# Kernel tuning notes

Hardware: AMD Instinct MI355X
Metric: run time of the kernel (lower is better)

The kernel has to match this reference:

```python
import jax, jax.numpy as jnp
import numpy as np

B, H, W = 64, 512, 512          # batch, image height/width
BH, BW = 8, 8                   # block_size
K = 256                         # n_blocks (codebook size)
L = BH * BW                     # block_len = 64
HT, WT = H // BH, W // BW       # tiles per axis
T = HT * WT                     # tiles_per_img = 4096
BETA = 35.0


def _unfold(img):
    # img: (B, 1, H, W) -> patches (B, T, L), matching torch.nn.Unfold
    # with kernel=stride=(BH,BW): tiles row-major, patch flattened (kh, kw).
    x = img.reshape(B, 1, HT, BH, WT, BW)
    x = x.transpose(0, 2, 4, 1, 3, 5)          # (B, HT, WT, 1, BH, BW)
    return x.reshape(B, T, L)


def _fold(patches):
    # patches: (B, T, L) -> img (B, 1, H, W); exact inverse of _unfold
    # (non-overlapping, so Fold is pure reassembly, no accumulation).
    x = patches.reshape(B, HT, WT, 1, BH, BW)
    x = x.transpose(0, 3, 1, 4, 2, 5)          # (B, 1, HT, BH, WT, BW)
    return x.reshape(B, 1, H, W)


def setup_inputs() -> dict:
    key = jax.random.key(0)
    k1, k2 = jax.random.split(key)
    target_img = jax.random.uniform(k1, (B, 1, H, W), dtype=jnp.float32)
    # Learned codebook parameter (Haar-ish init in the original; values
    # don't change the math being tested).
    blocks = jax.random.uniform(k2, (K, BH, BW), dtype=jnp.float32)
    return {"target_img": target_img, "blocks": blocks}


def reference(target_img, blocks):
    patches = _unfold(target_img).reshape(B * T, L)   # (N, L), N = B*T
    codes = blocks.reshape(K, L)                      # (K, L)

    # Squared distances ||a - b||^2 via the expanded form to avoid
    # materializing the (N, K, L) difference tensor.
    a2 = jnp.sum(patches * patches, axis=-1, keepdims=True)   # (N, 1)
    b2 = jnp.sum(codes * codes, axis=-1)                      # (K,)
    ab = patches @ codes.T                                    # (N, K)
    sqerr = a2 - 2.0 * ab + b2                                # (N, K)

    block_weights = jax.nn.softmax(-BETA * sqerr, axis=-1)    # (N, K)
    uf_reconstructed = block_weights @ codes                  # (N, L)

    reconstructed = _fold(uf_reconstructed.reshape(B, T, L))  # (B,1,H,W)
    choice_penalty = jnp.mean(
        jnp.minimum(block_weights, 1.0 - block_weights)) * K
    return reconstructed, choice_penalty
```

## Files before the change

kernel.cpp:

```cpp
#include <hip/hip_runtime.h>


namespace {
constexpr int   HALF   = 128;
constexpr float BETA_C = 35.0f;
constexpr float TAU    = 1e-6f;
constexpr int   NPATCH = 64 * 64 * 64;
constexpr size_t IMG_ELEMS = (size_t)64 * 512 * 512;
}

template <int H>
__device__ __forceinline__ void stage_codes(float* sC, const float* __restrict__ blk,
                                            int tid) {
#pragma unroll 8
  for (int i = 0; i < 32; ++i) {
    int f = i * 256 + tid;
    int kl = f >> 6;
    int d = f & 63;
    float v = blk[H * 8192 + f];
    sC[d * HALF + (kl ^ ((d & 15) << 1))] = v;
  }
}

template <int H>
__device__ __forceinline__ void gemm_half(float (&acc)[16][4], float (&b2acc)[4],
                                          const float* sC, const float* sP,
                                          int lane, int wave) {
  const float* prBase = &sP[wave * 16];
#pragma unroll 4
  for (int d = 0; d < 64; ++d) {
    const float2 c2 = *reinterpret_cast<const float2*>(
        &sC[d * HALF + 2 * (lane ^ (d & 15))]);
    b2acc[2 * H]     += c2.x * c2.x;
    b2acc[2 * H + 1] += c2.y * c2.y;
    const float* pr = prBase + d * 64;
#pragma unroll
    for (int pg = 0; pg < 4; ++pg) {
      const float4 pa = *reinterpret_cast<const float4*>(pr + pg * 4);
      acc[pg * 4 + 0][2 * H]     += pa.x * c2.x;
      acc[pg * 4 + 0][2 * H + 1] += pa.x * c2.y;
      acc[pg * 4 + 1][2 * H]     += pa.y * c2.x;
      acc[pg * 4 + 1][2 * H + 1] += pa.y * c2.y;
      acc[pg * 4 + 2][2 * H]     += pa.z * c2.x;
      acc[pg * 4 + 2][2 * H + 1] += pa.z * c2.y;
      acc[pg * 4 + 3][2 * H]     += pa.w * c2.x;
      acc[pg * 4 + 3][2 * H + 1] += pa.w * c2.y;
    }
  }
}

__global__ __launch_bounds__(256, 3) void recon_kernel(
    const float* __restrict__ img, const float* __restrict__ blk,
    float* __restrict__ out, float* __restrict__ penAcc) {
  __shared__ float sC[64 * HALF];
  __shared__ float sP[64 * 64];

  const int tid = threadIdx.x;
  const int lane = tid & 63;
  const int wave = tid >> 6;
  const int b = blockIdx.x >> 6;
  const int ht = blockIdx.x & 63;

  const float* imgBase = img + (size_t)b * (512 * 512) + (size_t)(ht * 8) * 512;
#pragma unroll
  for (int i = 0; i < 4; ++i) {
    int f4 = i * 256 + tid;
    int row = f4 >> 7;
    int c4 = f4 & 127;
    float4 v = reinterpret_cast<const float4*>(imgBase + row * 512)[c4];
    int col = c4 * 4;
    int wt = col >> 3;
    int dbase = row * 8 + (col & 7);
    sP[(dbase + 0) * 64 + wt] = v.x;
    sP[(dbase + 1) * 64 + wt] = v.y;
    sP[(dbase + 2) * 64 + wt] = v.z;
    sP[(dbase + 3) * 64 + wt] = v.w;
  }
  stage_codes<0>(sC, blk, tid);
  __syncthreads();

  float acc[16][4];
  float b2acc[4] = {0.f, 0.f, 0.f, 0.f};
#pragma unroll
  for (int p = 0; p < 16; ++p)
#pragma unroll
    for (int j = 0; j < 4; ++j) acc[p][j] = 0.f;

  gemm_half<0>(acc, b2acc, sC, sP, lane, wave);
  __syncthreads();
  stage_codes<1>(sC, blk, tid);
  __syncthreads();
  gemm_half<1>(acc, b2acc, sC, sP, lane, wave);

  float pen = 0.f;
  const int wtBase = wave * 16;
  const int kh = lane >> 3, kw = lane & 7;
  float* outRowBase =
      out + (size_t)b * (512 * 512) + (size_t)(ht * 8 + kh) * 512 + kw;

  for (int p = 0; p < 16; ++p) {
    float l0 = BETA_C * (2.f * acc[p][0] - b2acc[0]);
    float l1 = BETA_C * (2.f * acc[p][1] - b2acc[1]);
    float l2 = BETA_C * (2.f * acc[p][2] - b2acc[2]);
    float l3 = BETA_C * (2.f * acc[p][3] - b2acc[3]);
    float m = fmaxf(fmaxf(l0, l1), fmaxf(l2, l3));
#pragma unroll
    for (int off = 32; off >= 1; off >>= 1)
      m = fmaxf(m, __shfl_xor(m, off, 64));
    float e0 = __expf(l0 - m), e1 = __expf(l1 - m);
    float e2 = __expf(l2 - m), e3 = __expf(l3 - m);
    float s = (e0 + e1) + (e2 + e3);
#pragma unroll
    for (int off = 32; off >= 1; off >>= 1) s += __shfl_xor(s, off, 64);
    float inv = 1.0f / s;
    float w0 = e0 * inv, w1 = e1 * inv, w2 = e2 * inv, w3 = e3 * inv;
    pen += fmaxf(2.f * w0 - 1.f, 0.f) + fmaxf(2.f * w1 - 1.f, 0.f) +
           fmaxf(2.f * w2 - 1.f, 0.f) + fmaxf(2.f * w3 - 1.f, 0.f);

    bool flag = (w0 > TAU) || (w1 > TAU) || (w2 > TAU) || (w3 > TAU);
    unsigned long long mask = __ballot(flag ? 1 : 0);
    float r = 0.f;
    while (mask) {
      int L = __builtin_ctzll(mask);
      mask &= (mask - 1);
      float q0 = __shfl(w0, L, 64);
      float q1 = __shfl(w1, L, 64);
      float q2 = __shfl(w2, L, 64);
      float q3 = __shfl(w3, L, 64);
      const float* cb = blk + (2 * L) * 64 + lane;
      if (q0 > TAU) r = fmaf(q0, cb[0], r);
      if (q1 > TAU) r = fmaf(q1, cb[64], r);
      if (q2 > TAU) r = fmaf(q2, cb[HALF * 64], r);
      if (q3 > TAU) r = fmaf(q3, cb[HALF * 64 + 64], r);
    }
    outRowBase[(wtBase + p) * 8] = r;
  }

#pragma unroll
  for (int off = 32; off >= 1; off >>= 1) pen += __shfl_xor(pen, off, 64);
  if (lane == 0) atomicAdd(penAcc, pen);
}

__global__ void finalize_kernel(float* penSlot) {
  *penSlot = 1.0f - (*penSlot) * (1.0f / (float)NPATCH);
}

extern "C" void kernel_launch(void* const* d_in, const int* in_sizes, int n_in,
                              void* d_out, int out_size, void* d_ws, size_t ws_size,
                              hipStream_t stream) {
  const float* img = (const float*)d_in[0];
  const float* blk = (const float*)d_in[1];
  float* out = (float*)d_out;
  float* penSlot = out + IMG_ELEMS;

  hipMemsetAsync(penSlot, 0, sizeof(float), stream);
  recon_kernel<<<dim3(4096), dim3(256), 0, stream>>>(img, blk, out, penSlot);
  finalize_kernel<<<dim3(1), dim3(1), 0, stream>>>(penSlot);
}
```

Before: 406.5 us.

## Compute patch-codebook distances with split-bf16 MFMA and stage output through LDS

Replaces the scalar FP32 FMA distance GEMM with bf16 MFMA 16x16x32 instructions, splitting both operands into hi and lo bf16 parts to keep close to FP32 accuracy (hi*hi, lo*hi, hi*lo and lo*lo terms). A small pre-kernel packs the codebook into hi/lo bf16 fragments and precomputes the code norms, removing that work from each block. Softmax weights are written to shared memory as bf16, and the reconstructed patches are staged in shared memory so the image is written with coalesced float4 stores. The risk is reduced precision from storing the weights in bf16, plus extra LDS traffic and synchronisation.

```diff
diff --git a/kernel.cpp b/kernel.cpp
--- a/kernel.cpp
+++ b/kernel.cpp
@@ -1,148 +1,238 @@
 #include <hip/hip_runtime.h>
-
+#include <hip/hip_fp16.h>
+
+
+typedef short short8 __attribute__((ext_vector_type(8)));
+typedef float floatx4 __attribute__((ext_vector_type(4)));
 
 namespace {
-constexpr int   HALF   = 128;
 constexpr float BETA_C = 35.0f;
 constexpr float TAU    = 1e-6f;
-constexpr int   NPATCH = 64 * 64 * 64;
+constexpr float INV_N  = 1.0f / 262144.0f;
 constexpr size_t IMG_ELEMS = (size_t)64 * 512 * 512;
-}
-
-template <int H>
-__device__ __forceinline__ void stage_codes(float* sC, const float* __restrict__ blk,
-                                            int tid) {
-#pragma unroll 8
-  for (int i = 0; i < 32; ++i) {
-    int f = i * 256 + tid;
-    int kl = f >> 6;
-    int d = f & 63;
-    float v = blk[H * 8192 + f];
-    sC[d * HALF + (kl ^ ((d & 15) << 1))] = v;
-  }
-}
-
-template <int H>
-__device__ __forceinline__ void gemm_half(float (&acc)[16][4], float (&b2acc)[4],
-                                          const float* sC, const float* sP,
-                                          int lane, int wave) {
-  const float* prBase = &sP[wave * 16];
-#pragma unroll 4
-  for (int d = 0; d < 64; ++d) {
-    const float2 c2 = *reinterpret_cast<const float2*>(
-        &sC[d * HALF + 2 * (lane ^ (d & 15))]);
-    b2acc[2 * H]     += c2.x * c2.x;
-    b2acc[2 * H + 1] += c2.y * c2.y;
-    const float* pr = prBase + d * 64;
-#pragma unroll
-    for (int pg = 0; pg < 4; ++pg) {
-      const float4 pa = *reinterpret_cast<const float4*>(pr + pg * 4);
-      acc[pg * 4 + 0][2 * H]     += pa.x * c2.x;
-      acc[pg * 4 + 0][2 * H + 1] += pa.x * c2.y;
-      acc[pg * 4 + 1][2 * H]     += pa.y * c2.x;
-      acc[pg * 4 + 1][2 * H + 1] += pa.y * c2.y;
-      acc[pg * 4 + 2][2 * H]     += pa.z * c2.x;
-      acc[pg * 4 + 2][2 * H + 1] += pa.z * c2.y;
-      acc[pg * 4 + 3][2 * H]     += pa.w * c2.x;
-      acc[pg * 4 + 3][2 * H + 1] += pa.w * c2.y;
-    }
-  }
+constexpr int WB   = 0;
+constexpr int WA_H = 9216;
+constexpr int WA_L = 11264;
+constexpr int WW   = 0;
+constexpr int WR   = 8448;
+constexpr int NWORDS = 13312;
+}
+
+__device__ __forceinline__ unsigned short f2bf(float x) {
+  unsigned u = __float_as_uint(x);
+  return (unsigned short)((u + 0x7FFFu + ((u >> 16) & 1u)) >> 16);
+}
+__device__ __forceinline__ float bf2f(unsigned short h) {
+  return __uint_as_float((unsigned)h << 16);
+}
+__device__ __forceinline__ unsigned pack2(unsigned short lo, unsigned short hi) {
+  return (unsigned)lo | ((unsigned)hi << 16);
+}
+
+__global__ void pack_codes(const float* __restrict__ blk,
+                           unsigned* __restrict__ wsBh,
+                           unsigned* __restrict__ wsBl,
+                           float* __restrict__ wsB2) {
+  const int c = threadIdx.x;
+  const float* src = blk + c * 64;
+  float b2 = 0.f;
+#pragma unroll
+  for (int g = 0; g < 8; ++g) {
+#pragma unroll
+    for (int t = 0; t < 4; ++t) {
+      float v0 = src[g * 8 + 2 * t], v1 = src[g * 8 + 2 * t + 1];
+      b2 += v0 * v0 + v1 * v1;
+      unsigned short h0 = f2bf(v0), h1 = f2bf(v1);
+      unsigned short l0 = f2bf(v0 - bf2f(h0)), l1 = f2bf(v1 - bf2f(h1));
+      wsBh[(c * 8 + g) * 4 + t] = pack2(h0, h1);
+      wsBl[(c * 8 + g) * 4 + t] = pack2(l0, l1);
+    }
+  }
+  wsB2[c] = b2;
 }
 
 __global__ __launch_bounds__(256, 3) void recon_kernel(
     const float* __restrict__ img, const float* __restrict__ blk,
-    float* __restrict__ out, float* __restrict__ penAcc) {
-  __shared__ float sC[64 * HALF];
-  __shared__ float sP[64 * 64];
+    const unsigned* __restrict__ wsBh, const unsigned* __restrict__ wsBl,
+    const float* __restrict__ wsB2, float* __restrict__ out,
+    float* __restrict__ penAcc) {
+  __shared__ unsigned sMem[NWORDS];
+  float* sMemF = reinterpret_cast<float*>(sMem);
 
   const int tid = threadIdx.x;
   const int lane = tid & 63;
   const int wave = tid >> 6;
   const int b = blockIdx.x >> 6;
   const int ht = blockIdx.x & 63;
-
+  const int c15 = lane & 15;
+  const int q = lane >> 4;
+
+  {
+    const uint4* src = reinterpret_cast<const uint4*>(wsBh);
+#pragma unroll
+    for (int i = 0; i < 8; ++i) {
+      int j = i * 256 + tid;
+      *reinterpret_cast<uint4*>(&sMem[WB + (j + (j >> 3)) * 4]) = src[j];
+    }
+  }
   const float* imgBase = img + (size_t)b * (512 * 512) + (size_t)(ht * 8) * 512;
 #pragma unroll
   for (int i = 0; i < 4; ++i) {
     int f4 = i * 256 + tid;
-    int row = f4 >> 7;
-    int c4 = f4 & 127;
+    int row = f4 >> 7, c4 = f4 & 127;
     float4 v = reinterpret_cast<const float4*>(imgBase + row * 512)[c4];
-    int col = c4 * 4;
-    int wt = col >> 3;
-    int dbase = row * 8 + (col & 7);
-    sP[(dbase + 0) * 64 + wt] = v.x;
-    sP[(dbase + 1) * 64 + wt] = v.y;
-    sP[(dbase + 2) * 64 + wt] = v.z;
-    sP[(dbase + 3) * 64 + wt] = v.w;
-  }
-  stage_codes<0>(sC, blk, tid);
-  __syncthreads();
-
-  float acc[16][4];
-  float b2acc[4] = {0.f, 0.f, 0.f, 0.f};
-#pragma unroll
-  for (int p = 0; p < 16; ++p)
-#pragma unroll
-    for (int j = 0; j < 4; ++j) acc[p][j] = 0.f;
-
-  gemm_half<0>(acc, b2acc, sC, sP, lane, wave);
-  __syncthreads();
-  stage_codes<1>(sC, blk, tid);
-  __syncthreads();
-  gemm_half<1>(acc, b2acc, sC, sP, lane, wave);
+    int wt = c4 >> 1, hw = c4 & 1;
+    unsigned short h0 = f2bf(v.x), h1 = f2bf(v.y), h2 = f2bf(v.z), h3 = f2bf(v.w);
+    unsigned short l0 = f2bf(v.x - bf2f(h0)), l1 = f2bf(v.y - bf2f(h1));
+    unsigned short l2 = f2bf(v.z - bf2f(h2)), l3 = f2bf(v.w - bf2f(h3));
+    int base = wt * 32 + row * 4 + hw * 2;
+    *reinterpret_cast<uint2*>(&sMem[WA_H + base]) =
+        make_uint2(pack2(h0, h1), pack2(h2, h3));
+    *reinterpret_cast<uint2*>(&sMem[WA_L + base]) =
+        make_uint2(pack2(l0, l1), pack2(l2, l3));
+  }
+  __syncthreads();
+
+  const int patch = wave * 16 + c15;
+  short8 ah[2], al[2];
+#pragma unroll
+  for (int s = 0; s < 2; ++s) {
+    int base = patch * 32 + (4 * s + q) * 4;
+    ah[s] = *reinterpret_cast<const short8*>(&sMem[WA_H + base]);
+    al[s] = *reinterpret_cast<const short8*>(&sMem[WA_L + base]);
+  }
+
+  floatx4 acc[16];
+#pragma unroll
+  for (int n = 0; n < 16; ++n) acc[n] = (floatx4){0.f, 0.f, 0.f, 0.f};
+
+#pragma unroll
+  for (int n = 0; n < 16; ++n) {
+    const unsigned* pb = &sMem[WB + (144 * n + 9 * c15 + q) * 4];
+    short8 b0 = *reinterpret_cast<const short8*>(pb);
+    short8 b1 = *reinterpret_cast<const short8*>(pb + 16);
+    acc[n] = __builtin_amdgcn_mfma_f32_16x16x32_bf16(ah[0], b0, acc[n], 0, 0, 0);
+    acc[n] = __builtin_amdgcn_mfma_f32_16x16x32_bf16(al[0], b0, acc[n], 0, 0, 0);
+    acc[n] = __builtin_amdgcn_mfma_f32_16x16x32_bf16(ah[1], b1, acc[n], 0, 0, 0);
+    acc[n] = __builtin_amdgcn_mfma_f32_16x16x32_bf16(al[1], b1, acc[n], 0, 0, 0);
+  }
+  __syncthreads();
+  {
+    const uint4* src = reinterpret_cast<const uint4*>(wsBl);
+#pragma unroll
+    for (int i = 0; i < 8; ++i) {
+      int j = i * 256 + tid;
+      *reinterpret_cast<uint4*>(&sMem[WB + (j + (j >> 3)) * 4]) = src[j];
+    }
+  }
+  __syncthreads();
+#pragma unroll
+  for (int n = 0; n < 16; ++n) {
+    const unsigned* pb = &sMem[WB + (144 * n + 9 * c15 + q) * 4];
+    short8 b0 = *reinterpret_cast<const short8*>(pb);
+    short8 b1 = *reinterpret_cast<const short8*>(pb + 16);
+    acc[n] = __builtin_amdgcn_mfma_f32_16x16x32_bf16(ah[0], b0, acc[n], 0, 0, 0);
+    acc[n] = __builtin_amdgcn_mfma_f32_16x16x32_bf16(al[0], b0, acc[n], 0, 0, 0);
+    acc[n] = __builtin_amdgcn_mfma_f32_16x16x32_bf16(ah[1], b1, acc[n], 0, 0, 0);
+    acc[n] = __builtin_amdgcn_mfma_f32_16x16x32_bf16(al[1], b1, acc[n], 0, 0, 0);
+  }
+
+#pragma unroll
+  for (int n = 0; n < 16; ++n) {
+    float b2v = wsB2[16 * n + c15];
+#pragma unroll
+    for (int r = 0; r < 4; ++r)
+      acc[n][r] = fmaf(2.0f * BETA_C, acc[n][r], -BETA_C * b2v);
+  }
+  float mx[4], sm[4];
+#pragma unroll
+  for (int r = 0; r < 4; ++r) {
+    float m = acc[0][r];
+#pragma unroll
+    for (int n = 1; n < 16; ++n) m = fmaxf(m, acc[n][r]);
+#pragma unroll
+    for (int off = 1; off <= 8; off <<= 1) m = fmaxf(m, __shfl_xor(m, off, 64));
+    mx[r] = m;
+    sm[r] = 0.f;
+  }
+#pragma unroll
+  for (int n = 0; n < 16; ++n)
+#pragma unroll
+    for (int r = 0; r < 4; ++r) {
+      acc[n][r] = __expf(acc[n][r] - mx[r]);
+      sm[r] += acc[n][r];
+    }
+#pragma unroll
+  for (int r = 0; r < 4; ++r) {
+#pragma unroll
+    for (int off = 1; off <= 8; off <<= 1) sm[r] += __shfl_xor(sm[r], off, 64);
+    sm[r] = 1.0f / sm[r];
+  }
+
+  __syncthreads();
 
   float pen = 0.f;
-  const int wtBase = wave * 16;
-  const int kh = lane >> 3, kw = lane & 7;
-  float* outRowBase =
-      out + (size_t)b * (512 * 512) + (size_t)(ht * 8 + kh) * 512 + kw;
-
-  for (int p = 0; p < 16; ++p) {
-    float l0 = BETA_C * (2.f * acc[p][0] - b2acc[0]);
-    float l1 = BETA_C * (2.f * acc[p][1] - b2acc[1]);
-    float l2 = BETA_C * (2.f * acc[p][2] - b2acc[2]);
-    float l3 = BETA_C * (2.f * acc[p][3] - b2acc[3]);
-    float m = fmaxf(fmaxf(l0, l1), fmaxf(l2, l3));
-#pragma unroll
-    for (int off = 32; off >= 1; off >>= 1)
-      m = fmaxf(m, __shfl_xor(m, off, 64));
-    float e0 = __expf(l0 - m), e1 = __expf(l1 - m);
-    float e2 = __expf(l2 - m), e3 = __expf(l3 - m);
-    float s = (e0 + e1) + (e2 + e3);
-#pragma unroll
-    for (int off = 32; off >= 1; off >>= 1) s += __shfl_xor(s, off, 64);
-    float inv = 1.0f / s;
-    float w0 = e0 * inv, w1 = e1 * inv, w2 = e2 * inv, w3 = e3 * inv;
-    pen += fmaxf(2.f * w0 - 1.f, 0.f) + fmaxf(2.f * w1 - 1.f, 0.f) +
-           fmaxf(2.f * w2 - 1.f, 0.f) + fmaxf(2.f * w3 - 1.f, 0.f);
-
+#pragma unroll
+  for (int n = 0; n < 16; ++n)
+#pragma unroll
+    for (int r = 0; r < 4; ++r) {
+      float w = acc[n][r] * sm[r];
+      pen += fminf(w, 1.0f - w);
+      float wp = __shfl_xor(w, 1, 64);
+      if (!(c15 & 1)) {
+        int p = wave * 16 + 4 * q + r;
+        sMem[WW + p * 132 + 8 * n + (c15 >> 1)] = pack2(f2bf(w), f2bf(wp));
+      }
+    }
+#pragma unroll
+  for (int off = 1; off <= 32; off <<= 1) pen += __shfl_xor(pen, off, 64);
+  if (lane == 0) atomicAdd(penAcc, pen);
+
+#pragma unroll 1
+  for (int pl = 0; pl < 16; ++pl) {
+    int p = wave * 16 + pl;
+    unsigned u0 = sMem[WW + p * 132 + lane];
+    unsigned u1 = sMem[WW + p * 132 + 64 + lane];
+    float w0 = bf2f((unsigned short)(u0 & 0xFFFFu));
+    float w1 = bf2f((unsigned short)(u0 >> 16));
+    float w2 = bf2f((unsigned short)(u1 & 0xFFFFu));
+    float w3 = bf2f((unsigned short)(u1 >> 16));
     bool flag = (w0 > TAU) || (w1 > TAU) || (w2 > TAU) || (w3 > TAU);
-    unsigned long long mask = __ballot(flag ? 1 : 0);
-    float r = 0.f;
-    while (mask) {
-      int L = __builtin_ctzll(mask);
-      mask &= (mask - 1);
-      float q0 = __shfl(w0, L, 64);
-      float q1 = __shfl(w1, L, 64);
-      float q2 = __shfl(w2, L, 64);
-      float q3 = __shfl(w3, L, 64);
-      const float* cb = blk + (2 * L) * 64 + lane;
-      if (q0 > TAU) r = fmaf(q0, cb[0], r);
-      if (q1 > TAU) r = fmaf(q1, cb[64], r);
-      if (q2 > TAU) r = fmaf(q2, cb[HALF * 64], r);
-      if (q3 > TAU) r = fmaf(q3, cb[HALF * 64 + 64], r);
-    }
-    outRowBase[(wtBase + p) * 8] = r;
-  }
-
-#pragma unroll
-  for (int off = 32; off >= 1; off >>= 1) pen += __shfl_xor(pen, off, 64);
-  if (lane == 0) atomicAdd(penAcc, pen);
+    unsigned long long msk = __ballot(flag);
+    float rr = 0.f;
+    while (msk) {
+      int L = __builtin_ctzll(msk);
+      msk &= msk - 1;
+      unsigned a0 = (unsigned)__shfl((int)u0, L, 64);
+      unsigned a1 = (unsigned)__shfl((int)u1, L, 64);
+      float p0 = bf2f((unsigned short)(a0 & 0xFFFFu));
+      float p1 = bf2f((unsigned short)(a0 >> 16));
+      float p2 = bf2f((unsigned short)(a1 & 0xFFFFu));
+      float p3 = bf2f((unsigned short)(a1 >> 16));
+      const float* cb = blk + 2 * L * 64 + lane;
+      if (p0 > TAU) rr = fmaf(p0, cb[0], rr);
+      if (p1 > TAU) rr = fmaf(p1, cb[64], rr);
+      if (p2 > TAU) rr = fmaf(p2, cb[128 * 64], rr);
+      if (p3 > TAU) rr = fmaf(p3, cb[128 * 64 + 64], rr);
+    }
+    sMemF[WR + p * 68 + lane] = rr;
+  }
+  __syncthreads();
+
+  float* outBase = out + (size_t)b * (512 * 512) + (size_t)(ht * 8) * 512;
+#pragma unroll
+  for (int i = 0; i < 4; ++i) {
+    int f4 = i * 256 + tid;
+    int row = f4 >> 7, c4 = f4 & 127;
+    int wt = c4 >> 1, hw = c4 & 1;
+    float4 v = *reinterpret_cast<const float4*>(
+        &sMemF[WR + wt * 68 + row * 8 + hw * 4]);
+    reinterpret_cast<float4*>(outBase + row * 512)[c4] = v;
+  }
 }
 
 __global__ void finalize_kernel(float* penSlot) {
-  *penSlot = 1.0f - (*penSlot) * (1.0f / (float)NPATCH);
+  *penSlot = (*penSlot) * INV_N;
 }
 
 extern "C" void kernel_launch(void* const* d_in, const int* in_sizes, int n_in,
@@ -153,7 +243,13 @@
   float* out = (float*)d_out;
   float* penSlot = out + IMG_ELEMS;
 
+  unsigned* wsBh = (unsigned*)d_ws;
+  unsigned* wsBl = wsBh + 8192;
+  float* wsB2 = (float*)(wsBl + 8192);
+
+  pack_codes<<<dim3(1), dim3(256), 0, stream>>>(blk, wsBh, wsBl, wsB2);
   hipMemsetAsync(penSlot, 0, sizeof(float), stream);
-  recon_kernel<<<dim3(4096), dim3(256), 0, stream>>>(img, blk, out, penSlot);
+  recon_kernel<<<dim3(4096), dim3(256), 0, stream>>>(img, blk, wsBh, wsBl,
+                                                     wsB2, out, penSlot);
   finalize_kernel<<<dim3(1), dim3(1), 0, stream>>>(penSlot);
 }
```

Result: faster. 360.1 us (-11.4%).
